# Optimization experiments

Hardware: AMD Instinct MI355X
Metric: run time of the kernel (lower is better)

## Reference

```python
import jax, jax.numpy as jnp
import numpy as np

B, L = 4, 2048
D_MODEL, D_INNER, D_STATE, DT_RANK, D_CONV = 1024, 2048, 16, 64, 4


def setup_inputs() -> dict:
    key = jax.random.key(0)
    ks = jax.random.split(key, 10)
    s = lambda k, shape, sc: jax.random.normal(k, shape, dtype=jnp.float32) * sc
    return {
        "x": s(ks[0], (B, L, D_MODEL), 1.0),
        "W_in": s(ks[1], (2 * D_INNER, D_MODEL), D_MODEL ** -0.5),
        "conv_w": s(ks[2], (D_INNER, D_CONV), D_CONV ** -0.5),
        "conv_b": s(ks[3], (D_INNER,), 0.02),
        "A_log": jnp.log(jnp.arange(1, D_STATE + 1, dtype=jnp.float32)),
        "D": jnp.ones((D_INNER,), dtype=jnp.float32),
        "W_x": s(ks[4], (DT_RANK + 2 * D_STATE, D_INNER), D_INNER ** -0.5),
        "W_dt": s(ks[5], (D_INNER, DT_RANK), DT_RANK ** -0.5),
        "b_dt": s(ks[6], (D_INNER,), 0.02) - 4.0,  # softplus -> small positive dt
        "W_out": s(ks[7], (D_MODEL, D_INNER), D_INNER ** -0.5),
    }


def reference(x, W_in, conv_w, conv_b, A_log, D, W_x, W_dt, b_dt, W_out):
    Bb, Ll, _ = x.shape
    # input projection, split into ssm branch and gate branch
    xz = x @ W_in.T                       # (B, L, 2*Di)
    xr, z = jnp.split(xz, 2, axis=-1)     # (B, L, Di) each
    # depthwise causal conv1d (torch pads both sides then slices [:L])
    xc = jax.lax.conv_general_dilated(
        xr.transpose(0, 2, 1),            # (B, Di, L)
        conv_w[:, None, :],               # (Di, 1, K)
        window_strides=(1,),
        padding=[(D_CONV - 1, 0)],
        dimension_numbers=("NCH", "OIH", "NCH"),
        feature_group_count=D_INNER,
    ) + conv_b[None, :, None]
    xs = jax.nn.silu(xc.transpose(0, 2, 1))  # (B, L, Di)
    # input-dependent dt, B, C
    x_dbl = xs @ W_x.T                        # (B, L, dt_rank + 2*S)
    dt_r, b_sel, c_sel = jnp.split(x_dbl, [DT_RANK, DT_RANK + D_STATE], axis=-1)
    dt = jax.nn.softplus(dt_r @ W_dt.T + b_dt)  # (B, L, Di)
    a_diag = -jnp.exp(A_log)                    # (S,)

    def step(h, inp):
        dt_t, b_t, c_t, x_t = inp                       # (B,Di),(B,S),(B,S),(B,Di)
        a_bar = jnp.exp(dt_t[:, :, None] * a_diag)      # (B, Di, S)
        h = a_bar * h + (dt_t * x_t)[:, :, None] * b_t[:, None, :]
        y = jnp.einsum("bds,bs->bd", h, c_t) + D * x_t
        return h, y

    h0 = jnp.zeros((Bb, D_INNER, D_STATE), dtype=x.dtype)
    _, ys = jax.lax.scan(
        step, h0,
        (dt.transpose(1, 0, 2), b_sel.transpose(1, 0, 2),
         c_sel.transpose(1, 0, 2), xs.transpose(1, 0, 2)),
    )
    y = ys.transpose(1, 0, 2)                           # (B, L, Di)
    return (y * jax.nn.silu(z)) @ W_out.T               # (B, L, d_model)
```

## Files before the change

### kernel.cpp

```cpp
#include <hip/hip_runtime.h>
#include <math.h>

typedef unsigned short u16;
typedef unsigned int u32;

constexpr int Bb = 4, Ll = 2048, DM = 1024, DI = 2048, DS = 16, DTR = 64, KC = 4;
constexpr int M = Bb * Ll;
constexpr int NPAD = 128;
constexpr int NCHUNK = 32;
constexpr int LC = Ll / NCHUNK;
constexpr int LDXZ = 4096;

__device__ __forceinline__ float b2f(u16 u) {
    return __uint_as_float(((u32)u) << 16);
}
__device__ __forceinline__ u16 f2b(float f) {
    u32 x = __float_as_uint(f);
    u32 r = (x + 0x7fffu + ((x >> 16) & 1u)) >> 16;
    return (u16)r;
}

typedef __attribute__((ext_vector_type(8))) short short8;
typedef __attribute__((ext_vector_type(4))) short short4v;
typedef __attribute__((ext_vector_type(4))) float floatx4;

__device__ __forceinline__ void gload16(const u16* g, u16* l) {
    __builtin_amdgcn_global_load_lds(
        (const __attribute__((address_space(1))) void*)g,
        (__attribute__((address_space(3))) void*)l,
        16, 0, 0);
}

__device__ __forceinline__ void pow_tree(float a, float* aa) {
    float a2 = a * a, a4 = a2 * a2, a8 = a4 * a4;
    aa[0] = a;        aa[1] = a2;       aa[2] = a * a2;   aa[3] = a4;
    aa[4] = a * a4;   aa[5] = a2 * a4;  aa[6] = aa[2] * a4; aa[7] = a8;
    aa[8] = a * a8;   aa[9] = a2 * a8;  aa[10] = aa[2] * a8; aa[11] = a4 * a8;
    aa[12] = aa[4] * a8; aa[13] = aa[5] * a8; aa[14] = aa[6] * a8; aa[15] = a8 * a8;
}

template<int GX, int GY>
__device__ __forceinline__ void xcd_swizzle(int& bx, int& by) {
    const int bid = blockIdx.y * GX + blockIdx.x;
    const int xcd = bid & 7;
    const int i = bid >> 3;
    const int c_local = i >> 5;
    const int within = i & 31;
    const int lx = within & 7, ly = within >> 3;
    const int chunk = xcd + c_local * 8;
    constexpr int CXN = GX / 8;
    const int cx = chunk % CXN;
    const int cy = chunk / CXN;
    bx = cx * 8 + lx;
    by = cy * 4 + ly;
}

template<int OUTM>
__global__ __launch_bounds__(512, 2) void gemm256(
    const u16* __restrict__ A, const u16* __restrict__ Bm,
    void* __restrict__ Cv,
    int K, int lda, int ldb, int ldc)
{
    __shared__ alignas(16) u16 ldsA[4][256 * 32];
    __shared__ alignas(16) u16 ldsB[4][256 * 32];

    int bx, by;
    xcd_swizzle<16, 32>(bx, by);

    const int lane = threadIdx.x & 63;
    const int wave = threadIdx.x >> 6;
    const int wr = wave >> 2;
    const int wc = wave & 3;
    const int m0 = by * 256;
    const int n0 = bx * 256;

    const int lrow = lane >> 2;
    const int skc  = (((lane & 3) + (lane >> 3)) & 3) * 8;
    const u16* pA = A  + (size_t)(m0 + wave * 32 + lrow) * lda + skc;
    const u16* pB = Bm + (size_t)(n0 + wave * 32 + lrow) * ldb + skc;
    const int ldst = wave * 1024;

    const int r16 = lane & 15;
    const int quad = lane >> 4;
    const int slot = (quad + 4 - ((r16 >> 1) & 3)) & 3;
    const int aoff = (wr * 128 + r16) * 32 + slot * 8;
    const int boff = (wc * 64  + r16) * 32 + slot * 8;

    const int NT = K >> 5;

    floatx4 acc[8][4] = {};

#pragma unroll
    for (int t = 0; t < 3; ++t) {
        gload16(pA + t * 32,            &ldsA[t][ldst]);
        gload16(pA + t * 32 + 16 * lda, &ldsA[t][ldst + 512]);
        gload16(pB + t * 32,            &ldsB[t][ldst]);
        gload16(pB + t * 32 + 16 * ldb, &ldsB[t][ldst + 512]);
    }
    asm volatile("s_waitcnt vmcnt(8)" ::: "memory");
    __builtin_amdgcn_sched_barrier(0);
    __builtin_amdgcn_s_barrier();

    for (int t = 0; t < NT; ++t) {
        const u16* la = &ldsA[t & 3][aoff];
        const u16* lb = &ldsB[t & 3][boff];
        short8 af[8], bf[4];
#pragma unroll
        for (int i = 0; i < 8; ++i) af[i] = *(const short8*)(la + i * 512);
#pragma unroll
        for (int j = 0; j < 4; ++j) bf[j] = *(const short8*)(lb + j * 512);
        if (t + 3 < NT) {
            const u16* sA = pA + (t + 3) * 32;
            const u16* sB = pB + (t + 3) * 32;
            u16* dA = &ldsA[(t + 3) & 3][ldst];
            u16* dB = &ldsB[(t + 3) & 3][ldst];
            gload16(sA, dA);
            gload16(sA + 16 * lda, dA + 512);
            gload16(sB, dB);
            gload16(sB + 16 * ldb, dB + 512);
        }
        __builtin_amdgcn_sched_barrier(0);
        __builtin_amdgcn_s_barrier();
        asm volatile("s_waitcnt lgkmcnt(0)" ::: "memory");
        __builtin_amdgcn_sched_barrier(0);
        __builtin_amdgcn_s_setprio(1);
#pragma unroll
        for (int i = 0; i < 8; ++i)
#pragma unroll
            for (int j = 0; j < 4; ++j)
                acc[i][j] = __builtin_amdgcn_mfma_f32_16x16x32_bf16(
                    af[i], bf[j], acc[i][j], 0, 0, 0);
        __builtin_amdgcn_s_setprio(0);
        if (t + 3 < NT)      asm volatile("s_waitcnt vmcnt(8)" ::: "memory");
        else if (t + 2 < NT) asm volatile("s_waitcnt vmcnt(4)" ::: "memory");
        else if (t + 1 < NT) asm volatile("s_waitcnt vmcnt(0)" ::: "memory");
        __builtin_amdgcn_sched_barrier(0);
        __builtin_amdgcn_s_barrier();
    }

    const int mw = m0 + wr * 128;
    const int nw = n0 + wc * 64;
    const int rb = quad * 4;
#pragma unroll
    for (int i = 0; i < 8; ++i) {
#pragma unroll
        for (int j = 0; j < 4; ++j) {
            const int n = nw + j * 16 + r16;
#pragma unroll
            for (int r = 0; r < 4; ++r) {
                const int m = mw + i * 16 + rb + r;
                float v = acc[i][j][r];
                if (OUTM == 1)
                    ((float*)Cv)[(size_t)m * ldc + n] = v;
                else
                    ((u16*)Cv)[(size_t)m * ldc + n] = f2b(v);
            }
        }
    }
}

template<int OUTM>
__global__ __launch_bounds__(512, 4) void gemm256n128(
    const u16* __restrict__ A, const u16* __restrict__ Bm,
    void* __restrict__ Cv,
    int K, int lda, int ldb, int ldc)
{
    __shared__ alignas(16) u16 ldsA[3][256 * 32];
    __shared__ alignas(16) u16 ldsB[3][128 * 32];

    int bx, by;
    xcd_swizzle<8, 32>(bx, by);

    const int lane = threadIdx.x & 63;
    const int wave = threadIdx.x >> 6;
    const int wr = wave >> 1;
    const int wc = wave & 1;
    const int m0 = by * 256;
    const int n0 = bx * 128;

    const int lrow = lane >> 2;
    const int skc  = (((lane & 3) + (lane >> 3)) & 3) * 8;
    const u16* pA = A  + (size_t)(m0 + wave * 32 + lrow) * lda + skc;
    const u16* pB = Bm + (size_t)(n0 + wave * 16 + lrow) * ldb + skc;
    const int ldstA = wave * 1024;
    const int ldstB = wave * 512;

    const int r16 = lane & 15;
    const int quad = lane >> 4;
    const int slot = (quad + 4 - ((r16 >> 1) & 3)) & 3;
    const int aoff = (wr * 64 + r16) * 32 + slot * 8;
    const int boff = (wc * 64 + r16) * 32 + slot * 8;

    const int NT = K >> 5;

    floatx4 acc[4][4] = {};

#pragma unroll
    for (int t = 0; t < 2; ++t) {
        gload16(pA + t * 32,            &ldsA[t][ldstA]);
        gload16(pA + t * 32 + 16 * lda, &ldsA[t][ldstA + 512]);
        gload16(pB + t * 32,            &ldsB[t][ldstB]);
    }
    asm volatile("s_waitcnt vmcnt(3)" ::: "memory");
    __builtin_amdgcn_sched_barrier(0);
    __builtin_amdgcn_s_barrier();

    int bc = 0, bs = 2;
    for (int t = 0; t < NT; ++t) {
        const u16* la = &ldsA[bc][aoff];
        const u16* lb = &ldsB[bc][boff];
        short8 af[4], bf[4];
#pragma unroll
        for (int i = 0; i < 4; ++i) af[i] = *(const short8*)(la + i * 512);
#pragma unroll
        for (int j = 0; j < 4; ++j) bf[j] = *(const short8*)(lb + j * 512);
        if (t + 2 < NT) {
            const u16* sa = pA + (t + 2) * 32;
            u16* da = &ldsA[bs][ldstA];
            gload16(sa, da);
            gload16(sa + 16 * lda, da + 512);
            gload16(pB + (t + 2) * 32, &ldsB[bs][ldstB]);
        }
        __builtin_amdgcn_sched_barrier(0);
        __builtin_amdgcn_s_barrier();
        asm volatile("s_waitcnt lgkmcnt(0)" ::: "memory");
        __builtin_amdgcn_sched_barrier(0);
        __builtin_amdgcn_s_setprio(1);
#pragma unroll
        for (int i = 0; i < 4; ++i)
#pragma unroll
            for (int j = 0; j < 4; ++j)
                acc[i][j] = __builtin_amdgcn_mfma_f32_16x16x32_bf16(
                    af[i], bf[j], acc[i][j], 0, 0, 0);
        __builtin_amdgcn_s_setprio(0);
        if (t + 2 < NT)      asm volatile("s_waitcnt vmcnt(3)" ::: "memory");
        else if (t + 1 < NT) asm volatile("s_waitcnt vmcnt(0)" ::: "memory");
        __builtin_amdgcn_sched_barrier(0);
        __builtin_amdgcn_s_barrier();
        bc = (bc == 2) ? 0 : bc + 1;
        bs = (bs == 2) ? 0 : bs + 1;
    }

    const int mw = m0 + wr * 64;
    const int nw = n0 + wc * 64;
    const int rb = quad * 4;
#pragma unroll
    for (int i = 0; i < 4; ++i) {
#pragma unroll
        for (int j = 0; j < 4; ++j) {
            const int n = nw + j * 16 + r16;
#pragma unroll
            for (int r = 0; r < 4; ++r) {
                const int m = mw + i * 16 + rb + r;
                float v = acc[i][j][r];
                if (OUTM == 1)
                    ((float*)Cv)[(size_t)m * ldc + n] = v;
                else
                    ((u16*)Cv)[(size_t)m * ldc + n] = f2b(v);
            }
        }
    }
}

template<int OUTM>
__global__ __launch_bounds__(256) void gemm_bt(
    const u16* __restrict__ A, const u16* __restrict__ Bm,
    void* __restrict__ Cv, const float* __restrict__ bias,
    int K, int lda, int ldb, int ldc)
{
    __shared__ alignas(16) u16 ldsA[128 * 32];
    __shared__ alignas(16) u16 ldsB[128 * 32];

    const int lane = threadIdx.x & 63;
    const int wave = threadIdx.x >> 6;
    const int wr = wave >> 1, wc = wave & 1;
    const int m0 = blockIdx.y * 128;
    const int n0 = blockIdx.x * 128;
    const int koff = (OUTM == 4) ? blockIdx.z * K : 0;

    const int srow = wave * 32 + (lane >> 2);
    const int skc  = (((lane & 3) + (lane >> 3)) & 3) * 8;
    const u16* Ag = A + (size_t)(m0 + srow) * lda + skc + koff;
    const u16* Bg = Bm + (size_t)(n0 + srow) * ldb + skc + koff;
    u16* lA = &ldsA[wave * 1024];
    u16* lB = &ldsB[wave * 1024];

    const int r16 = lane & 15;
    const int quad = lane >> 4;
    const int slot = (quad + 4 - ((r16 >> 1) & 3)) & 3;
    const u16* arow = &ldsA[(wr * 64 + r16) * 32 + slot * 8];
    const u16* brow = &ldsB[(wc * 64 + r16) * 32 + slot * 8];

    floatx4 acc[4][4] = {};

    for (int k0 = 0; k0 < K; k0 += 32) {
        gload16(Ag + k0,                    lA);
        gload16(Ag + k0 + (size_t)16 * lda, lA + 512);
        gload16(Bg + k0,                    lB);
        gload16(Bg + k0 + (size_t)16 * ldb, lB + 512);
        __syncthreads();

        short8 af[4], bf[4];
#pragma unroll
        for (int i = 0; i < 4; i++) af[i] = *(const short8*)(arow + i * 16 * 32);
#pragma unroll
        for (int j = 0; j < 4; j++) bf[j] = *(const short8*)(brow + j * 16 * 32);
#pragma unroll
        for (int i = 0; i < 4; i++)
#pragma unroll
            for (int j = 0; j < 4; j++)
                acc[i][j] = __builtin_amdgcn_mfma_f32_16x16x32_bf16(
                    af[i], bf[j], acc[i][j], 0, 0, 0);
        __syncthreads();
    }

    const int mw = m0 + wr * 64;
    const int nw = n0 + wc * 64;
    const int rb = quad * 4;
#pragma unroll
    for (int i = 0; i < 4; i++) {
#pragma unroll
        for (int j = 0; j < 4; j++) {
            const int n = nw + j * 16 + r16;
#pragma unroll
            for (int r = 0; r < 4; r++) {
                const int m = mw + i * 16 + rb + r;
                float v = acc[i][j][r];
                if (OUTM == 2) {
                    v += bias[n];
                    v = (v > 20.f) ? v : log1pf(__expf(v));
                }
                if (OUTM == 4)
                    ((float*)Cv)[((size_t)blockIdx.z * M + m) * ldc + n] = v;
                else if (OUTM == 1)
                    ((float*)Cv)[(size_t)m * ldc + n] = v;
                else
                    ((u16*)Cv)[(size_t)m * ldc + n] = f2b(v);
            }
        }
    }
}

__global__ __launch_bounds__(256) void redk_gemm3(
    const float* __restrict__ part, u16* __restrict__ xdbl,
    float* __restrict__ bcf)
{
    const int t = blockIdx.x * 256 + threadIdx.x;
    const int c4 = t % 24;
    const int m = t / 24;
    const int n4 = c4 * 4;
    const size_t stride = (size_t)M * NPAD;
    const float* p = part + (size_t)m * NPAD + n4;
    floatx4 acc = *(const floatx4*)(p)
                + *(const floatx4*)(p + stride)
                + *(const floatx4*)(p + 2 * stride)
                + *(const floatx4*)(p + 3 * stride);
    if (n4 < 64) {
        short4v ob;
#pragma unroll
        for (int j = 0; j < 4; j++) ob[j] = (short)f2b(acc[j]);
        *(short4v*)(xdbl + (size_t)m * 64 + n4) = ob;
    } else {
        *(floatx4*)(bcf + (size_t)m * 32 + (n4 - 64)) = acc;
    }
}

__global__ __launch_bounds__(256) void prep_all(
    const float* __restrict__ x, const float* __restrict__ W_in,
    const float* __restrict__ W_x, const float* __restrict__ W_dt,
    const float* __restrict__ W_out,
    u16* __restrict__ xbf, u16* __restrict__ wibf, u16* __restrict__ wxp,
    u16* __restrict__ wdtb, u16* __restrict__ woutb)
{
    constexpr int N0 = M * DM;
    constexpr int N1 = 2 * DI * DM;
    constexpr int N2 = NPAD * DI;
    constexpr int N3 = DI * DTR;
    int idx = blockIdx.x * blockDim.x + threadIdx.x;
    if (idx < N0) {
        xbf[idx] = f2b(x[idx]);
        return;
    }
    idx -= N0;
    if (idx < N1) {
        wibf[idx] = f2b(W_in[idx]);
    } else if (idx < N1 + N2) {
        int i = idx - N1;
        int r = i >> 11, c = i & 2047;
        wxp[i] = (r < 96) ? f2b(W_x[r * 2048 + c]) : (u16)0;
    } else if (idx < N1 + N2 + N3) {
        int i = idx - N1 - N2;
        wdtb[i] = f2b(W_dt[i]);
    } else {
        int i = idx - N1 - N2 - N3;
        woutb[i] = f2b(W_out[i]);
    }
}

__global__ __launch_bounds__(256) void conv_silu(
    const u16* __restrict__ xz, const float* __restrict__ conv_w,
    const float* __restrict__ conv_b, u16* __restrict__ xs)
{
    const int m = blockIdx.x;
    const int d0 = threadIdx.x * 8;
    const int l = m & (Ll - 1);

    float acc[8];
    {
        floatx4 cb0 = *(const floatx4*)(conv_b + d0);
        floatx4 cb1 = *(const floatx4*)(conv_b + d0 + 4);
#pragma unroll
        for (int j = 0; j < 4; j++) { acc[j] = cb0[j]; acc[4 + j] = cb1[j]; }
    }
    float w[8][KC];
#pragma unroll
    for (int jd = 0; jd < 8; jd++) {
        floatx4 wv = *(const floatx4*)(conv_w + (d0 + jd) * KC);
#pragma unroll
        for (int k = 0; k < KC; k++) w[jd][k] = wv[k];
    }
#pragma unroll
    for (int k = 0; k < KC; k++) {
        int li = l - (KC - 1) + k;
        if (li >= 0) {
            short8 xv = *(const short8*)(xz + (size_t)(m - (KC - 1) + k) * LDXZ + d0);
#pragma unroll
            for (int jd = 0; jd < 8; jd++)
                acc[jd] += b2f((u16)xv[jd]) * w[jd][k];
        }
    }
    short8 o;
#pragma unroll
    for (int jd = 0; jd < 8; jd++) {
        float s = acc[jd] / (1.f + __expf(-acc[jd]));
        o[jd] = (short)f2b(s);
    }
    *(short8*)(xs + (size_t)m * DI + d0) = o;
}

__global__ __launch_bounds__(256) void scan_p1(
    const u16* __restrict__ xzdt, const u16* __restrict__ xs,
    const float* __restrict__ bcf, const float* __restrict__ A_log,
    float* __restrict__ scr_h, float* __restrict__ sdt_g)
{
    __shared__ alignas(16) float bcs[LC * 32];

    const int d = blockIdx.x * 256 + threadIdx.x;
    const int b = blockIdx.y;
    const int c = blockIdx.z;
    const int m0 = b * Ll + c * LC;

    {
        const float* bc_g = bcf + (size_t)m0 * 32;
#pragma unroll
        for (int j = 0; j < 2; j++) {
            int idx = j * 1024 + threadIdx.x * 4;
            *(floatx4*)(bcs + idx) = *(const floatx4*)(bc_g + idx);
        }
    }

    const float ad0 = -__expf(A_log[0]);
    float adl[DS];
    bool fast = true;
#pragma unroll
    for (int s = 0; s < DS; s++) {
        float av = -__expf(A_log[s]);
        adl[s] = av;
        float kr = (float)(s + 1);
        if (fabsf(av / ad0 - kr) > 1e-4f * kr) fast = false;
    }

    const u16* dt_p = xzdt + (size_t)m0 * LDXZ + d;
    const u16* xs_p = xs + (size_t)m0 * DI + d;

    float h[DS] = {};
    float sdt = 0.f;

    __syncthreads();

    u16 dt_c = dt_p[0],     xs_c = xs_p[0];
    u16 dt_1 = dt_p[LDXZ],  xs_1 = xs_p[DI];

    if (fast) {
        for (int l = 0; l < LC; l++) {
            u16 dt_2 = dt_p[2 * LDXZ];
            u16 xs_2 = xs_p[2 * DI];
            const float* bl = bcs + l * 32;
            floatx4 B0 = *(const floatx4*)(bl);
            floatx4 B1 = *(const floatx4*)(bl + 4);
            floatx4 B2 = *(const floatx4*)(bl + 8);
            floatx4 B3 = *(const floatx4*)(bl + 12);

            float dtv = b2f(dt_c);
            float xv  = b2f(xs_c);
            float bx = dtv * xv;
            sdt += dtv;
            float aa[DS];
            pow_tree(__expf(dtv * ad0), aa);
#pragma unroll
            for (int s = 0; s < DS; s++) {
                float Bv = (s < 4) ? B0[s] : (s < 8) ? B1[s - 4]
                         : (s < 12) ? B2[s - 8] : B3[s - 12];
                h[s] = aa[s] * h[s] + bx * Bv;
            }
            dt_c = dt_1; dt_1 = dt_2; xs_c = xs_1; xs_1 = xs_2;
            dt_p += LDXZ; xs_p += DI;
        }
    } else {
        for (int l = 0; l < LC; l++) {
            u16 dt_2 = dt_p[2 * LDXZ];
            u16 xs_2 = xs_p[2 * DI];
            const float* bl = bcs + l * 32;
            floatx4 B0 = *(const floatx4*)(bl);
            floatx4 B1 = *(const floatx4*)(bl + 4);
            floatx4 B2 = *(const floatx4*)(bl + 8);
            floatx4 B3 = *(const floatx4*)(bl + 12);

            float dtv = b2f(dt_c);
            float xv  = b2f(xs_c);
            float bx = dtv * xv;
            sdt += dtv;
#pragma unroll
            for (int s = 0; s < DS; s++) {
                float Bv = (s < 4) ? B0[s] : (s < 8) ? B1[s - 4]
                         : (s < 12) ? B2[s - 8] : B3[s - 12];
                float a = __expf(dtv * adl[s]);
                h[s] = a * h[s] + bx * Bv;
            }
            dt_c = dt_1; dt_1 = dt_2; xs_c = xs_1; xs_1 = xs_2;
            dt_p += LDXZ; xs_p += DI;
        }
    }

    const size_t base = ((size_t)(b * NCHUNK + c) * DI + d) * DS;
#pragma unroll
    for (int s = 0; s < DS; s += 4) {
        floatx4 hv = {h[s], h[s+1], h[s+2], h[s+3]};
        *(floatx4*)(scr_h + base + s) = hv;
    }
    sdt_g[(size_t)(b * NCHUNK + c) * DI + d] = sdt;
}

__global__ __launch_bounds__(256) void scan_p2(
    float* __restrict__ scr_h, const float* __restrict__ sdt_g,
    const float* __restrict__ A_log)
{
    const int t = blockIdx.x * 256 + threadIdx.x;
    const int s = t & 15;
    const int d = (t >> 4) & (DI - 1);
    const int b = t >> 15;
    const float adl = -__expf(A_log[s]);

    float he[NCHUNK], P[NCHUNK];
#pragma unroll
    for (int c = 0; c < NCHUNK; c++) {
        const size_t base = ((size_t)(b * NCHUNK + c) * DI + d) * DS + s;
        he[c] = scr_h[base];
        P[c] = adl * sdt_g[(size_t)(b * NCHUNK + c) * DI + d];
    }
#pragma unroll
    for (int c = 0; c < NCHUNK; c++) P[c] = __expf(P[c]);
    float hin = 0.f;
#pragma unroll
    for (int c = 0; c < NCHUNK; c++) {
        const size_t base = ((size_t)(b * NCHUNK + c) * DI + d) * DS + s;
        scr_h[base] = hin;
        hin = P[c] * hin + he[c];
    }
}

__global__ __launch_bounds__(256) void scan_p3(
    const u16* __restrict__ xz, const u16* xs, const float* __restrict__ bcf,
    const float* __restrict__ scr_hin, const float* __restrict__ A_log,
    const float* __restrict__ Dvec, u16* yg)
{
    __shared__ alignas(16) float bcs[LC * 32];

    const int d = blockIdx.x * 256 + threadIdx.x;
    const int b = blockIdx.y;
    const int c = blockIdx.z;
    const int m0 = b * Ll + c * LC;

    {
        const float* bc_g = bcf + (size_t)m0 * 32;
#pragma unroll
        for (int j = 0; j < 2; j++) {
            int idx = j * 1024 + threadIdx.x * 4;
            *(floatx4*)(bcs + idx) = *(const floatx4*)(bc_g + idx);
        }
    }

    const float ad0 = -__expf(A_log[0]);
    float adl[DS];
    bool fast = true;
#pragma unroll
    for (int s = 0; s < DS; s++) {
        float av = -__expf(A_log[s]);
        adl[s] = av;
        float kr = (float)(s + 1);
        if (fabsf(av / ad0 - kr) > 1e-4f * kr) fast = false;
    }
    const float Dd = Dvec[d];

    const u16* dt_p = xz + (size_t)m0 * LDXZ + d;
    const u16* z_p  = xz + (size_t)m0 * LDXZ + 2048 + d;
    const u16* xs_p = xs + (size_t)m0 * DI + d;
    u16* yg_p = yg + (size_t)m0 * DI + d;

    float h[DS];
    const size_t base = ((size_t)(b * NCHUNK + c) * DI + d) * DS;
#pragma unroll
    for (int s = 0; s < DS; s += 4) {
        floatx4 hv = *(const floatx4*)(scr_hin + base + s);
        h[s] = hv[0]; h[s+1] = hv[1]; h[s+2] = hv[2]; h[s+3] = hv[3];
    }

    __syncthreads();

    u16 dt_c = dt_p[0],    dt_1 = dt_p[LDXZ];
    u16 xs_c = xs_p[0],    xs_1 = xs_p[DI];
    u16 z_c  = z_p[0],     z_1  = z_p[LDXZ];

    for (int l = 0; l < LC; l++) {
        u16 dt_2 = dt_p[2 * LDXZ];
        u16 xs_2 = xs_p[2 * DI];
        u16 z_2  = z_p[2 * LDXZ];
        const float* bl = bcs + l * 32;
        floatx4 Bq[4], Cq[4];
#pragma unroll
        for (int q = 0; q < 4; q++) {
            Bq[q] = *(const floatx4*)(bl + q * 4);
            Cq[q] = *(const floatx4*)(bl + 16 + q * 4);
        }

        float dtv = b2f(dt_c);
        float xv  = b2f(xs_c);
        float bx = dtv * xv;
        float aa[DS];
        if (fast) {
            pow_tree(__expf(dtv * ad0), aa);
        } else {
#pragma unroll
            for (int s = 0; s < DS; s++) aa[s] = __expf(dtv * adl[s]);
        }
        float y0 = 0.f, y1 = 0.f, y2 = 0.f, y3 = 0.f;
#pragma unroll
        for (int q = 0; q < 4; q++) {
#pragma unroll
            for (int j = 0; j < 4; j++) {
                int s = q * 4 + j;
                h[s] = aa[s] * h[s] + bx * Bq[q][j];
            }
        }
#pragma unroll
        for (int j = 0; j < 4; j++) {
            y0 += h[j] * Cq[0][j];
            y1 += h[4 + j] * Cq[1][j];
            y2 += h[8 + j] * Cq[2][j];
            y3 += h[12 + j] * Cq[3][j];
        }
        float yt = ((y0 + y1) + (y2 + y3)) + Dd * xv;
        float zv = b2f(z_c);
        float g = zv / (1.f + __expf(-zv));
        yg_p[0] = f2b(yt * g);

        dt_c = dt_1; dt_1 = dt_2;
        xs_c = xs_1; xs_1 = xs_2;
        z_c  = z_1;  z_1  = z_2;
        dt_p += LDXZ; xs_p += DI; z_p += LDXZ; yg_p += DI;
    }
}

extern "C" void kernel_launch(void* const* d_in, const int* in_sizes, int n_in,
                              void* d_out, int out_size, void* d_ws, size_t ws_size,
                              hipStream_t stream)
{
    const float* x      = (const float*)d_in[0];
    const float* W_in   = (const float*)d_in[1];
    const float* conv_w = (const float*)d_in[2];
    const float* conv_b = (const float*)d_in[3];
    const float* A_log  = (const float*)d_in[4];
    const float* Dvec   = (const float*)d_in[5];
    const float* W_x    = (const float*)d_in[6];
    const float* W_dt   = (const float*)d_in[7];
    const float* b_dt   = (const float*)d_in[8];
    const float* W_out  = (const float*)d_in[9];

    u16* ws = (u16*)d_ws;
    u16* xz    = ws;                 ws += (size_t)M * LDXZ;
    u16* xs    = ws;                 ws += (size_t)M * DI;
    u16* xbf   = ws;                 ws += (size_t)M * DM;
    u16* wibf  = ws;                 ws += (size_t)2 * DI * DM;
    u16* wxp   = ws;                 ws += (size_t)NPAD * DI;
    u16* wdtb  = ws;                 ws += (size_t)DI * DTR;
    u16* woutb = ws;                 ws += (size_t)DM * DI;
    u16* xdbl  = ws;                 ws += (size_t)M * NPAD;
    u16* yg    = xs;
    float* part  = (float*)xbf;
    float* scr_h = (float*)xbf;
    float* bcf   = (float*)wibf;
    float* sdt_g = bcf + (size_t)M * 32;

    {
        constexpr int NTOT = M * DM + 2 * DI * DM + NPAD * DI + DI * DTR + DM * DI;
        prep_all<<<NTOT / 256, 256, 0, stream>>>(
            x, W_in, W_x, W_dt, W_out, xbf, wibf, wxp, wdtb, woutb);
    }

    gemm256<0><<<dim3(LDXZ / 256, M / 256), 512, 0, stream>>>(
        xbf, wibf, xz, DM, DM, DM, LDXZ);

    conv_silu<<<M, 256, 0, stream>>>(xz, conv_w, conv_b, xs);

    gemm_bt<4><<<dim3(1, M / 128, 4), 256, 0, stream>>>(
        xs, wxp, part, nullptr, DI / 4, DI, DI, NPAD);
    redk_gemm3<<<(M * 24) / 256, 256, 0, stream>>>(part, xdbl, bcf);

    gemm_bt<2><<<dim3(DI / 128, M / 128), 256, 0, stream>>>(
        xdbl, wdtb, xz, b_dt, DTR, 64, DTR, LDXZ);

    scan_p1<<<dim3(DI / 256, Bb, NCHUNK), 256, 0, stream>>>(
        xz, xs, bcf, A_log, scr_h, sdt_g);
    scan_p2<<<(Bb * DI * DS) / 256, 256, 0, stream>>>(scr_h, sdt_g, A_log);
    scan_p3<<<dim3(DI / 256, Bb, NCHUNK), 256, 0, stream>>>(
        xz, xs, bcf, scr_h, A_log, Dvec, yg);

    gemm256n128<1><<<dim3(DM / 128, M / 256), 512, 0, stream>>>(
        yg, woutb, d_out, DI, DI, DI, DM);
}
```

Baseline: 463.1 us.

## Fuse split-K reduction into gemm3 and chunk-prefix into scan phase 1 via last-block counters

The split-K x_dbl GEMM now counts finished K-slices per row tile with an atomic counter, and the last block to finish performs the reduction, so the separate redk kernel launch is gone. Scan phase 1 likewise uses per-(batch, column-block) counters so the last chunk block runs the inter-chunk prefix recurrence, removing the scan_p2 launch. Counters are zeroed inside prep_all. The cost is that the cross-chunk recurrence now runs in only 32 blocks with serial 16-wide work per thread, instead of a fully parallel kernel, and correctness depends on threadfence ordering.

```diff
diff --git a/kernel.cpp b/kernel.cpp
--- a/kernel.cpp
+++ b/kernel.cpp
@@ -276,12 +276,11 @@
     const int wr = wave >> 1, wc = wave & 1;
     const int m0 = blockIdx.y * 128;
     const int n0 = blockIdx.x * 128;
-    const int koff = (OUTM == 4) ? blockIdx.z * K : 0;
 
     const int srow = wave * 32 + (lane >> 2);
     const int skc  = (((lane & 3) + (lane >> 3)) & 3) * 8;
-    const u16* Ag = A + (size_t)(m0 + srow) * lda + skc + koff;
-    const u16* Bg = Bm + (size_t)(n0 + srow) * ldb + skc + koff;
+    const u16* Ag = A + (size_t)(m0 + srow) * lda + skc;
+    const u16* Bg = Bm + (size_t)(n0 + srow) * ldb + skc;
     u16* lA = &ldsA[wave * 1024];
     u16* lB = &ldsB[wave * 1024];
 
@@ -330,9 +329,7 @@
                     v += bias[n];
                     v = (v > 20.f) ? v : log1pf(__expf(v));
                 }
-                if (OUTM == 4)
-                    ((float*)Cv)[((size_t)blockIdx.z * M + m) * ldc + n] = v;
-                else if (OUTM == 1)
+                if (OUTM == 1)
                     ((float*)Cv)[(size_t)m * ldc + n] = v;
                 else
                     ((u16*)Cv)[(size_t)m * ldc + n] = f2b(v);
@@ -341,27 +338,99 @@
     }
 }
 
-__global__ __launch_bounds__(256) void redk_gemm3(
-    const float* __restrict__ part, u16* __restrict__ xdbl,
-    float* __restrict__ bcf)
+__global__ __launch_bounds__(256) void gemm3_redk(
+    const u16* __restrict__ A, const u16* __restrict__ Bm,
+    float* __restrict__ part, u16* __restrict__ xdbl,
+    float* __restrict__ bcf, u32* __restrict__ ctr)
 {
-    const int t = blockIdx.x * 256 + threadIdx.x;
-    const int c4 = t % 24;
-    const int m = t / 24;
-    const int n4 = c4 * 4;
-    const size_t stride = (size_t)M * NPAD;
-    const float* p = part + (size_t)m * NPAD + n4;
-    floatx4 acc = *(const floatx4*)(p)
-                + *(const floatx4*)(p + stride)
-                + *(const floatx4*)(p + 2 * stride)
-                + *(const floatx4*)(p + 3 * stride);
-    if (n4 < 64) {
-        short4v ob;
-#pragma unroll
-        for (int j = 0; j < 4; j++) ob[j] = (short)f2b(acc[j]);
-        *(short4v*)(xdbl + (size_t)m * 64 + n4) = ob;
-    } else {
-        *(floatx4*)(bcf + (size_t)m * 32 + (n4 - 64)) = acc;
+    __shared__ alignas(16) u16 ldsA[128 * 32];
+    __shared__ alignas(16) u16 ldsB[128 * 32];
+    __shared__ int amLast;
+
+    const int lane = threadIdx.x & 63;
+    const int wave = threadIdx.x >> 6;
+    const int wr = wave >> 1, wc = wave & 1;
+    const int m0 = blockIdx.y * 128;
+    constexpr int K = DI / 4;
+    const int koff = blockIdx.z * K;
+
+    const int srow = wave * 32 + (lane >> 2);
+    const int skc  = (((lane & 3) + (lane >> 3)) & 3) * 8;
+    const u16* Ag = A + (size_t)(m0 + srow) * DI + skc + koff;
+    const u16* Bg = Bm + (size_t)srow * DI + skc + koff;
+    u16* lA = &ldsA[wave * 1024];
+    u16* lB = &ldsB[wave * 1024];
+
+    const int r16 = lane & 15;
+    const int quad = lane >> 4;
+    const int slot = (quad + 4 - ((r16 >> 1) & 3)) & 3;
+    const u16* arow = &ldsA[(wr * 64 + r16) * 32 + slot * 8];
+    const u16* brow = &ldsB[(wc * 64 + r16) * 32 + slot * 8];
+
+    floatx4 acc[4][4] = {};
+
+    for (int k0 = 0; k0 < K; k0 += 32) {
+        gload16(Ag + k0,                   lA);
+        gload16(Ag + k0 + (size_t)16 * DI, lA + 512);
+        gload16(Bg + k0,                   lB);
+        gload16(Bg + k0 + (size_t)16 * DI, lB + 512);
+        __syncthreads();
+
+        short8 af[4], bf[4];
+#pragma unroll
+        for (int i = 0; i < 4; i++) af[i] = *(const short8*)(arow + i * 16 * 32);
+#pragma unroll
+        for (int j = 0; j < 4; j++) bf[j] = *(const short8*)(brow + j * 16 * 32);
+#pragma unroll
+        for (int i = 0; i < 4; i++)
+#pragma unroll
+            for (int j = 0; j < 4; j++)
+                acc[i][j] = __builtin_amdgcn_mfma_f32_16x16x32_bf16(
+                    af[i], bf[j], acc[i][j], 0, 0, 0);
+        __syncthreads();
+    }
+
+    const int mw = m0 + wr * 64;
+    const int nw = wc * 64;
+    const int rb = quad * 4;
+#pragma unroll
+    for (int i = 0; i < 4; i++) {
+#pragma unroll
+        for (int j = 0; j < 4; j++) {
+            const int n = nw + j * 16 + r16;
+#pragma unroll
+            for (int r = 0; r < 4; r++) {
+                const int m = mw + i * 16 + rb + r;
+                part[((size_t)blockIdx.z * M + m) * NPAD + n] = acc[i][j][r];
+            }
+        }
+    }
+
+    __threadfence();
+    if (threadIdx.x == 0)
+        amLast = (atomicAdd(&ctr[blockIdx.y], 1u) == 3u);
+    __syncthreads();
+    if (!amLast) return;
+    __threadfence();
+
+    for (int it = threadIdx.x; it < 128 * 24; it += 256) {
+        const int r = it / 24;
+        const int n4 = (it - r * 24) * 4;
+        const int m = m0 + r;
+        const size_t stride = (size_t)M * NPAD;
+        const float* p = part + (size_t)m * NPAD + n4;
+        floatx4 a4 = *(const floatx4*)(p)
+                   + *(const floatx4*)(p + stride)
+                   + *(const floatx4*)(p + 2 * stride)
+                   + *(const floatx4*)(p + 3 * stride);
+        if (n4 < 64) {
+            short4v ob;
+#pragma unroll
+            for (int j = 0; j < 4; j++) ob[j] = (short)f2b(a4[j]);
+            *(short4v*)(xdbl + (size_t)m * 64 + n4) = ob;
+        } else {
+            *(floatx4*)(bcf + (size_t)m * 32 + (n4 - 64)) = a4;
+        }
     }
 }
 
@@ -370,12 +439,13 @@
     const float* __restrict__ W_x, const float* __restrict__ W_dt,
     const float* __restrict__ W_out,
     u16* __restrict__ xbf, u16* __restrict__ wibf, u16* __restrict__ wxp,
-    u16* __restrict__ wdtb, u16* __restrict__ woutb)
+    u16* __restrict__ wdtb, u16* __restrict__ woutb, u32* __restrict__ ctrs)
 {
     constexpr int N0 = M * DM;
     constexpr int N1 = 2 * DI * DM;
     constexpr int N2 = NPAD * DI;
     constexpr int N3 = DI * DTR;
+    if (blockIdx.x == 0 && threadIdx.x < 96) ctrs[threadIdx.x] = 0;
     int idx = blockIdx.x * blockDim.x + threadIdx.x;
     if (idx < N0) {
         xbf[idx] = f2b(x[idx]);
@@ -438,12 +508,14 @@
     *(short8*)(xs + (size_t)m * DI + d0) = o;
 }
 
-__global__ __launch_bounds__(256) void scan_p1(
+__global__ __launch_bounds__(256) void scan_p1p2(
     const u16* __restrict__ xzdt, const u16* __restrict__ xs,
     const float* __restrict__ bcf, const float* __restrict__ A_log,
-    float* __restrict__ scr_h, float* __restrict__ sdt_g)
+    float* __restrict__ scr_h, float* __restrict__ sdt_g,
+    u32* __restrict__ ctr2)
 {
     __shared__ alignas(16) float bcs[LC * 32];
+    __shared__ int last;
 
     const int d = blockIdx.x * 256 + threadIdx.x;
     const int b = blockIdx.y;
@@ -539,33 +611,45 @@
         *(floatx4*)(scr_h + base + s) = hv;
     }
     sdt_g[(size_t)(b * NCHUNK + c) * DI + d] = sdt;
-}
-
-__global__ __launch_bounds__(256) void scan_p2(
-    float* __restrict__ scr_h, const float* __restrict__ sdt_g,
-    const float* __restrict__ A_log)
-{
-    const int t = blockIdx.x * 256 + threadIdx.x;
-    const int s = t & 15;
-    const int d = (t >> 4) & (DI - 1);
-    const int b = t >> 15;
-    const float adl = -__expf(A_log[s]);
-
-    float he[NCHUNK], P[NCHUNK];
-#pragma unroll
-    for (int c = 0; c < NCHUNK; c++) {
-        const size_t base = ((size_t)(b * NCHUNK + c) * DI + d) * DS + s;
-        he[c] = scr_h[base];
-        P[c] = adl * sdt_g[(size_t)(b * NCHUNK + c) * DI + d];
-    }
-#pragma unroll
-    for (int c = 0; c < NCHUNK; c++) P[c] = __expf(P[c]);
-    float hin = 0.f;
-#pragma unroll
-    for (int c = 0; c < NCHUNK; c++) {
-        const size_t base = ((size_t)(b * NCHUNK + c) * DI + d) * DS + s;
-        scr_h[base] = hin;
-        hin = P[c] * hin + he[c];
+
+    __threadfence();
+    if (threadIdx.x == 0)
+        last = (atomicAdd(&ctr2[b * 8 + blockIdx.x], 1u) == (u32)(NCHUNK - 1));
+    __syncthreads();
+    if (!last) return;
+    __threadfence();
+
+    float hin[DS];
+#pragma unroll
+    for (int s = 0; s < DS; s++) hin[s] = 0.f;
+    for (int cc = 0; cc < NCHUNK; cc++) {
+        const size_t cb = ((size_t)(b * NCHUNK + cc) * DI + d) * DS;
+        const float sv = sdt_g[(size_t)(b * NCHUNK + cc) * DI + d];
+        float P[DS];
+        if (fast) {
+            pow_tree(__expf(ad0 * sv), P);
+        } else {
+#pragma unroll
+            for (int s = 0; s < DS; s++) P[s] = __expf(adl[s] * sv);
+        }
+        floatx4 he0 = *(const floatx4*)(scr_h + cb);
+        floatx4 he1 = *(const floatx4*)(scr_h + cb + 4);
+        floatx4 he2 = *(const floatx4*)(scr_h + cb + 8);
+        floatx4 he3 = *(const floatx4*)(scr_h + cb + 12);
+        floatx4 o0 = {hin[0], hin[1], hin[2], hin[3]};
+        floatx4 o1 = {hin[4], hin[5], hin[6], hin[7]};
+        floatx4 o2 = {hin[8], hin[9], hin[10], hin[11]};
+        floatx4 o3 = {hin[12], hin[13], hin[14], hin[15]};
+        *(floatx4*)(scr_h + cb)      = o0;
+        *(floatx4*)(scr_h + cb + 4)  = o1;
+        *(floatx4*)(scr_h + cb + 8)  = o2;
+        *(floatx4*)(scr_h + cb + 12) = o3;
+#pragma unroll
+        for (int s = 0; s < DS; s++) {
+            float he = (s < 4) ? he0[s] : (s < 8) ? he1[s - 4]
+                     : (s < 12) ? he2[s - 8] : he3[s - 12];
+            hin[s] = P[s] * hin[s] + he;
+        }
     }
 }
 
@@ -695,16 +779,16 @@
     u16* wdtb  = ws;                 ws += (size_t)DI * DTR;
     u16* woutb = ws;                 ws += (size_t)DM * DI;
     u16* xdbl  = ws;                 ws += (size_t)M * NPAD;
-    u16* yg    = xs;
     float* part  = (float*)xbf;
     float* scr_h = (float*)xbf;
     float* bcf   = (float*)wibf;
     float* sdt_g = bcf + (size_t)M * 32;
+    u32* ctrs   = (u32*)(xdbl + (size_t)M * 64);
 
     {
         constexpr int NTOT = M * DM + 2 * DI * DM + NPAD * DI + DI * DTR + DM * DI;
         prep_all<<<NTOT / 256, 256, 0, stream>>>(
-            x, W_in, W_x, W_dt, W_out, xbf, wibf, wxp, wdtb, woutb);
+            x, W_in, W_x, W_dt, W_out, xbf, wibf, wxp, wdtb, woutb, ctrs);
     }
 
     gemm256<0><<<dim3(LDXZ / 256, M / 256), 512, 0, stream>>>(
@@ -712,19 +796,18 @@
 
     conv_silu<<<M, 256, 0, stream>>>(xz, conv_w, conv_b, xs);
 
-    gemm_bt<4><<<dim3(1, M / 128, 4), 256, 0, stream>>>(
-        xs, wxp, part, nullptr, DI / 4, DI, DI, NPAD);
-    redk_gemm3<<<(M * 24) / 256, 256, 0, stream>>>(part, xdbl, bcf);
+    gemm3_redk<<<dim3(1, M / 128, 4), 256, 0, stream>>>(
+        xs, wxp, part, xdbl, bcf, ctrs);
 
     gemm_bt<2><<<dim3(DI / 128, M / 128), 256, 0, stream>>>(
         xdbl, wdtb, xz, b_dt, DTR, 64, DTR, LDXZ);
 
-    scan_p1<<<dim3(DI / 256, Bb, NCHUNK), 256, 0, stream>>>(
-        xz, xs, bcf, A_log, scr_h, sdt_g);
-    scan_p2<<<(Bb * DI * DS) / 256, 256, 0, stream>>>(scr_h, sdt_g, A_log);
+    scan_p1p2<<<dim3(DI / 256, Bb, NCHUNK), 256, 0, stream>>>(
+        xz, xs, bcf, A_log, scr_h, sdt_g, ctrs + 64);
+
     scan_p3<<<dim3(DI / 256, Bb, NCHUNK), 256, 0, stream>>>(
-        xz, xs, bcf, scr_h, A_log, Dvec, yg);
+        xz, xs, bcf, scr_h, A_log, Dvec, xs);
 
     gemm256n128<1><<<dim3(DM / 128, M / 256), 512, 0, stream>>>(
-        yg, woutb, d_out, DI, DI, DI, DM);
-}
+        xs, woutb, d_out, DI, DI, DI, DM);
+}
```

Result: slower. 675.5 us (+45.8%).

## Fuse split-K reduction into dt projection GEMM with softplus epilogue

Applied to the files above, without the earlier changes.

Replaces the separate split-K reduction kernel and the dt GEMM with one kernel. It sums the four fp32 partials directly into shared memory as bf16, runs a K=64 MFMA tile against W_dt, and applies bias plus softplus in the epilogue. The B/C columns are also reduced inside this kernel by the blocks with blockIdx.x 0. This removes one launch and the xdbl round trip, but every one of the 16 column blocks re-reduces the same partials, which adds redundant global reads. The partial GEMM now skips storing columns at or above 96, and scan_p2 moves to a rolled outer loop over chunk groups of 8 to cut register pressure.

```diff
diff --git a/kernel.cpp b/kernel.cpp
--- a/kernel.cpp
+++ b/kernel.cpp
@@ -322,14 +322,11 @@
 #pragma unroll
         for (int j = 0; j < 4; j++) {
             const int n = nw + j * 16 + r16;
+            if (OUTM == 4 && n >= 96) continue;
 #pragma unroll
             for (int r = 0; r < 4; r++) {
                 const int m = mw + i * 16 + rb + r;
                 float v = acc[i][j][r];
-                if (OUTM == 2) {
-                    v += bias[n];
-                    v = (v > 20.f) ? v : log1pf(__expf(v));
-                }
                 if (OUTM == 4)
                     ((float*)Cv)[((size_t)blockIdx.z * M + m) * ldc + n] = v;
                 else if (OUTM == 1)
@@ -341,27 +338,117 @@
     }
 }
 
-__global__ __launch_bounds__(256) void redk_gemm3(
-    const float* __restrict__ part, u16* __restrict__ xdbl,
+__global__ __launch_bounds__(256) void gemm4_fused(
+    const float* __restrict__ part, const u16* __restrict__ wdtb,
+    const float* __restrict__ b_dt, u16* __restrict__ xz,
     float* __restrict__ bcf)
 {
-    const int t = blockIdx.x * 256 + threadIdx.x;
-    const int c4 = t % 24;
-    const int m = t / 24;
-    const int n4 = c4 * 4;
-    const size_t stride = (size_t)M * NPAD;
-    const float* p = part + (size_t)m * NPAD + n4;
-    floatx4 acc = *(const floatx4*)(p)
-                + *(const floatx4*)(p + stride)
-                + *(const floatx4*)(p + 2 * stride)
-                + *(const floatx4*)(p + 3 * stride);
-    if (n4 < 64) {
-        short4v ob;
-#pragma unroll
-        for (int j = 0; j < 4; j++) ob[j] = (short)f2b(acc[j]);
-        *(short4v*)(xdbl + (size_t)m * 64 + n4) = ob;
-    } else {
-        *(floatx4*)(bcf + (size_t)m * 32 + (n4 - 64)) = acc;
+    __shared__ alignas(16) u16 lA[128 * 64];
+    __shared__ alignas(16) u16 lB[128 * 64];
+
+    const int tid = threadIdx.x;
+    const int m0 = blockIdx.y * 128;
+    const int n0 = blockIdx.x * 128;
+
+    {
+        const int r = tid >> 1;
+        const int hh = tid & 1;
+        const size_t stride = (size_t)M * NPAD;
+        const float* p = part + (size_t)(m0 + r) * NPAD + hh * 32;
+#pragma unroll
+        for (int cg = 0; cg < 4; cg++) {
+            floatx4 s0 = *(const floatx4*)(p + cg * 8)
+                       + *(const floatx4*)(p + stride + cg * 8)
+                       + *(const floatx4*)(p + 2 * stride + cg * 8)
+                       + *(const floatx4*)(p + 3 * stride + cg * 8);
+            floatx4 s1 = *(const floatx4*)(p + cg * 8 + 4)
+                       + *(const floatx4*)(p + stride + cg * 8 + 4)
+                       + *(const floatx4*)(p + 2 * stride + cg * 8 + 4)
+                       + *(const floatx4*)(p + 3 * stride + cg * 8 + 4);
+            short8 ob;
+#pragma unroll
+            for (int j = 0; j < 4; j++) {
+                ob[j]     = (short)f2b(s0[j]);
+                ob[4 + j] = (short)f2b(s1[j]);
+            }
+            const int g = hh * 4 + cg;
+            *(short8*)(&lA[r * 64 + ((g ^ (r & 7)) * 8)]) = ob;
+        }
+    }
+    {
+        const int rn = tid >> 1;
+        const int hh = tid & 1;
+        const u16* src = wdtb + (size_t)(n0 + rn) * 64 + hh * 32;
+#pragma unroll
+        for (int cg = 0; cg < 4; cg++) {
+            short8 wv = *(const short8*)(src + cg * 8);
+            const int g = hh * 4 + cg;
+            *(short8*)(&lB[rn * 64 + ((g ^ (rn & 7)) * 8)]) = wv;
+        }
+    }
+    if (blockIdx.x == 0) {
+        const int r = tid >> 1;
+        const int hh = tid & 1;
+        const size_t stride = (size_t)M * NPAD;
+        const float* p = part + (size_t)(m0 + r) * NPAD + 64 + hh * 16;
+        float* q = bcf + (size_t)(m0 + r) * 32 + hh * 16;
+#pragma unroll
+        for (int g = 0; g < 4; g++) {
+            floatx4 s = *(const floatx4*)(p + g * 4)
+                      + *(const floatx4*)(p + stride + g * 4)
+                      + *(const floatx4*)(p + 2 * stride + g * 4)
+                      + *(const floatx4*)(p + 3 * stride + g * 4);
+            *(floatx4*)(q + g * 4) = s;
+        }
+    }
+    __syncthreads();
+
+    const int lane = tid & 63;
+    const int wave = tid >> 6;
+    const int wr = wave >> 1, wc = wave & 1;
+    const int r16 = lane & 15;
+    const int quad = lane >> 4;
+
+    floatx4 acc[4][4] = {};
+#pragma unroll
+    for (int ks = 0; ks < 2; ks++) {
+        short8 af[4], bf[4];
+        const int g = ks * 4 + quad;
+#pragma unroll
+        for (int i = 0; i < 4; i++) {
+            const int row = wr * 64 + i * 16 + r16;
+            af[i] = *(const short8*)(&lA[row * 64 + ((g ^ (row & 7)) * 8)]);
+        }
+#pragma unroll
+        for (int j = 0; j < 4; j++) {
+            const int row = wc * 64 + j * 16 + r16;
+            bf[j] = *(const short8*)(&lB[row * 64 + ((g ^ (row & 7)) * 8)]);
+        }
+#pragma unroll
+        for (int i = 0; i < 4; i++)
+#pragma unroll
+            for (int j = 0; j < 4; j++)
+                acc[i][j] = __builtin_amdgcn_mfma_f32_16x16x32_bf16(
+                    af[i], bf[j], acc[i][j], 0, 0, 0);
+    }
+
+    const int mw = m0 + wr * 64;
+    const int nw = n0 + wc * 64;
+    const int rb = quad * 4;
+#pragma unroll
+    for (int i = 0; i < 4; i++) {
+#pragma unroll
+        for (int j = 0; j < 4; j++) {
+            const int n = nw + j * 16 + r16;
+            const float bb = b_dt[n];
+#pragma unroll
+            for (int r = 0; r < 4; r++) {
+                const int m = mw + i * 16 + rb + r;
+                float v = acc[i][j][r] + bb;
+                v = (v > 20.f) ? v : log1pf(__expf(v));
+                xz[(size_t)m * LDXZ + n] = f2b(v);
+            }
+        }
     }
 }
 
@@ -551,21 +638,23 @@
     const int b = t >> 15;
     const float adl = -__expf(A_log[s]);
 
-    float he[NCHUNK], P[NCHUNK];
-#pragma unroll
-    for (int c = 0; c < NCHUNK; c++) {
-        const size_t base = ((size_t)(b * NCHUNK + c) * DI + d) * DS + s;
-        he[c] = scr_h[base];
-        P[c] = adl * sdt_g[(size_t)(b * NCHUNK + c) * DI + d];
-    }
-#pragma unroll
-    for (int c = 0; c < NCHUNK; c++) P[c] = __expf(P[c]);
     float hin = 0.f;
-#pragma unroll
-    for (int c = 0; c < NCHUNK; c++) {
-        const size_t base = ((size_t)(b * NCHUNK + c) * DI + d) * DS + s;
-        scr_h[base] = hin;
-        hin = P[c] * hin + he[c];
+    for (int c0 = 0; c0 < NCHUNK; c0 += 8) {
+        float he[8], P[8];
+#pragma unroll
+        for (int j = 0; j < 8; j++) {
+            const size_t base = ((size_t)(b * NCHUNK + c0 + j) * DI + d) * DS + s;
+            he[j] = scr_h[base];
+            P[j] = adl * sdt_g[(size_t)(b * NCHUNK + c0 + j) * DI + d];
+        }
+#pragma unroll
+        for (int j = 0; j < 8; j++) P[j] = __expf(P[j]);
+#pragma unroll
+        for (int j = 0; j < 8; j++) {
+            const size_t base = ((size_t)(b * NCHUNK + c0 + j) * DI + d) * DS + s;
+            scr_h[base] = hin;
+            hin = P[j] * hin + he[j];
+        }
     }
 }
 
@@ -695,11 +784,11 @@
     u16* wdtb  = ws;                 ws += (size_t)DI * DTR;
     u16* woutb = ws;                 ws += (size_t)DM * DI;
     u16* xdbl  = ws;                 ws += (size_t)M * NPAD;
-    u16* yg    = xs;
     float* part  = (float*)xbf;
     float* scr_h = (float*)xbf;
     float* bcf   = (float*)wibf;
     float* sdt_g = bcf + (size_t)M * 32;
+    (void)xdbl;
 
     {
         constexpr int NTOT = M * DM + 2 * DI * DM + NPAD * DI + DI * DTR + DM * DI;
@@ -714,17 +803,16 @@
 
     gemm_bt<4><<<dim3(1, M / 128, 4), 256, 0, stream>>>(
         xs, wxp, part, nullptr, DI / 4, DI, DI, NPAD);
-    redk_gemm3<<<(M * 24) / 256, 256, 0, stream>>>(part, xdbl, bcf);
-
-    gemm_bt<2><<<dim3(DI / 128, M / 128), 256, 0, stream>>>(
-        xdbl, wdtb, xz, b_dt, DTR, 64, DTR, LDXZ);
+
+    gemm4_fused<<<dim3(DI / 128, M / 128), 256, 0, stream>>>(
+        part, wdtb, b_dt, xz, bcf);
 
     scan_p1<<<dim3(DI / 256, Bb, NCHUNK), 256, 0, stream>>>(
         xz, xs, bcf, A_log, scr_h, sdt_g);
     scan_p2<<<(Bb * DI * DS) / 256, 256, 0, stream>>>(scr_h, sdt_g, A_log);
     scan_p3<<<dim3(DI / 256, Bb, NCHUNK), 256, 0, stream>>>(
-        xz, xs, bcf, scr_h, A_log, Dvec, yg);
+        xz, xs, bcf, scr_h, A_log, Dvec, xs);
 
     gemm256n128<1><<<dim3(DM / 128, M / 256), 512, 0, stream>>>(
-        yg, woutb, d_out, DI, DI, DI, DM);
-}
+        xs, woutb, d_out, DI, DI, DI, DM);
+}
```

Measured after the change: 481.3 us. 1.04x slower.
